# Kernel tuning notes

Hardware: AMD Instinct MI355X
Metric: run time of the kernel (lower is better)

The kernel has to match this reference:

```python
import jax, jax.numpy as jnp
import numpy as np

EMB = 256
N_HEADS = 8
N_LVLS = 4
N_POINTS = 4
HEAD_DIM = EMB // N_HEADS  # 32
D_FFN = 1024
SHAPES = [(100, 100), (50, 50), (25, 25), (13, 13)]
LEN = sum(h * w for h, w in SHAPES)  # 13294
B = 4


def setup_inputs() -> dict:
    key = jax.random.key(0)
    ks = jax.random.split(key, 20)
    rn = lambda k, s, sc=0.02: jax.random.normal(k, s, jnp.float32) * sc
    starts = np.cumsum([0] + [h * w for h, w in SHAPES])[:-1]
    return {
        'features': jax.random.normal(ks[0], (B, LEN, EMB), jnp.float32),
        'pos': jax.random.normal(ks[1], (B, LEN, EMB), jnp.float32),
        'reference_points': jax.random.uniform(ks[2], (B, LEN, N_LVLS, 2), jnp.float32),
        'spatial_shapes': jnp.array(SHAPES, jnp.int32),
        'lvl_start_idx': jnp.array(starts, jnp.int32),
        'W_off': rn(ks[3], (EMB, N_HEADS * N_LVLS * N_POINTS * 2)),
        'b_off': rn(ks[4], (N_HEADS * N_LVLS * N_POINTS * 2,), 0.5),
        'W_attn': rn(ks[5], (EMB, N_HEADS * N_LVLS * N_POINTS)),
        'b_attn': rn(ks[6], (N_HEADS * N_LVLS * N_POINTS,)),
        'W_val': rn(ks[7], (EMB, EMB)),
        'b_val': rn(ks[8], (EMB,)),
        'W_out': rn(ks[9], (EMB, EMB)),
        'b_out': rn(ks[10], (EMB,)),
        'ln1_g': jnp.ones((EMB,), jnp.float32),
        'ln1_b': jnp.zeros((EMB,), jnp.float32),
        'W1': rn(ks[11], (EMB, D_FFN)),
        'b1': rn(ks[12], (D_FFN,)),
        'W2': rn(ks[13], (D_FFN, EMB)),
        'b2': rn(ks[14], (EMB,)),
        'ln2_g': jnp.ones((EMB,), jnp.float32),
        'ln2_b': jnp.zeros((EMB,), jnp.float32),
    }


def _layer_norm(x, g, b, eps=1e-5):
    mu = jnp.mean(x, axis=-1, keepdims=True)
    var = jnp.mean(jnp.square(x - mu), axis=-1, keepdims=True)
    return (x - mu) * jax.lax.rsqrt(var + eps) * g + b


def _ms_deform_attn(q, features, reference_points, shapes, starts,
                    W_off, b_off, W_attn, b_attn, W_val, b_val, W_out, b_out):
    Bn, Lq, D = features.shape
    value = (features @ W_val + b_val).reshape(Bn, Lq, N_HEADS, HEAD_DIM)
    off = (q @ W_off + b_off).reshape(Bn, Lq, N_HEADS, N_LVLS, N_POINTS, 2)
    attn = (q @ W_attn + b_attn).reshape(Bn, Lq, N_HEADS, N_LVLS * N_POINTS)
    attn = jax.nn.softmax(attn, axis=-1).reshape(Bn, Lq, N_HEADS, N_LVLS, N_POINTS)
    # normalizer per level is (W, H) for (x, y)
    norm = jnp.array([[w, h] for h, w in shapes], jnp.float32)  # (L, 2)
    loc = reference_points[:, :, None, :, None, :] + off / norm[None, None, None, :, None, :]

    out = jnp.zeros((Bn, N_HEADS, Lq, HEAD_DIM), value.dtype)
    for l, (H_, W_) in enumerate(shapes):
        s = starts[l]
        val = value[:, s:s + H_ * W_].transpose(0, 2, 1, 3)  # (B, nH, HW, Dh)
        locl = loc[:, :, :, l]  # (B, Lq, nH, P, 2), in [0,1]
        # grid_sample align_corners=False convention
        x = locl[..., 0] * W_ - 0.5
        y = locl[..., 1] * H_ - 0.5
        x0 = jnp.floor(x); y0 = jnp.floor(y)
        wx = x - x0; wy = y - y0
        x0i = x0.astype(jnp.int32); y0i = y0.astype(jnp.int32)

        def corner(xi, yi, w):
            valid = (xi >= 0) & (xi < W_) & (yi >= 0) & (yi < H_)
            idx = jnp.clip(yi, 0, H_ - 1) * W_ + jnp.clip(xi, 0, W_ - 1)  # (B, Lq, nH, P)
            idx = idx.transpose(0, 2, 1, 3).reshape(Bn, N_HEADS, Lq * N_POINTS, 1)
            g = jnp.take_along_axis(val, idx, axis=2)  # (B, nH, Lq*P, Dh)
            wm = (w * valid.astype(w.dtype)).transpose(0, 2, 1, 3).reshape(Bn, N_HEADS, Lq * N_POINTS, 1)
            return g * wm

        samp = (corner(x0i, y0i, (1 - wx) * (1 - wy))
                + corner(x0i + 1, y0i, wx * (1 - wy))
                + corner(x0i, y0i + 1, (1 - wx) * wy)
                + corner(x0i + 1, y0i + 1, wx * wy))
        samp = samp.reshape(Bn, N_HEADS, Lq, N_POINTS, HEAD_DIM)
        aw = attn[:, :, :, l].transpose(0, 2, 1, 3)  # (B, nH, Lq, P)
        out = out + jnp.einsum('bhqpd,bhqp->bhqd', samp, aw)

    out = out.transpose(0, 2, 1, 3).reshape(Bn, Lq, D)
    return out @ W_out + b_out


def reference(features, pos, reference_points, spatial_shapes, lvl_start_idx,
              W_off, b_off, W_attn, b_attn, W_val, b_val, W_out, b_out,
              ln1_g, ln1_b, W1, b1, W2, b2, ln2_g, ln2_b):
    shapes = [tuple(int(v) for v in r) for r in np.asarray(spatial_shapes)]
    starts = [int(v) for v in np.asarray(lvl_start_idx)]
    q = features + pos
    attn_out = _ms_deform_attn(q, features, reference_points, shapes, starts,
                               W_off, b_off, W_attn, b_attn, W_val, b_val, W_out, b_out)
    x = _layer_norm(features + attn_out, ln1_g, ln1_b)  # dropout is identity in eval
    ffn = jax.nn.relu(x @ W1 + b1) @ W2 + b2
    x = _layer_norm(x + ffn, ln2_g, ln2_b)  # stochastic depth is identity in eval
    return x
```

## Files before the change

kernel.cpp:

```cpp
#include <hip/hip_runtime.h>
#include <stdint.h>

#define LEN_T 13294
#define M_TOK 53176

typedef unsigned short u16;
typedef __bf16 bf16x8 __attribute__((ext_vector_type(8)));
typedef float f32x4 __attribute__((ext_vector_type(4)));
typedef uint32_t u32x4 __attribute__((ext_vector_type(4)));

__device__ __forceinline__ u16 f2bf(float f) {
    union { float f; uint32_t u; } v; v.f = f;
    uint32_t r = v.u + 0x7fffu + ((v.u >> 16) & 1u);
    return (u16)(r >> 16);
}
__device__ __forceinline__ float bf2f(u16 s) {
    union { uint32_t u; float f; } v; v.u = ((uint32_t)s) << 16;
    return v.f;
}
__device__ __forceinline__ u16 f2h(float f) {
    union { _Float16 h; u16 u; } c; c.h = (_Float16)f; return c.u;
}
__device__ __forceinline__ float hlo(uint32_t u) {
    union { uint32_t u; _Float16 h[2]; } v; v.u = u; return (float)v.h[0];
}
__device__ __forceinline__ float hhi(uint32_t u) {
    union { uint32_t u; _Float16 h[2]; } v; v.u = u; return (float)v.h[1];
}

__device__ __forceinline__ void gload_lds16(const u16* g, u16* l) {
    __builtin_amdgcn_global_load_lds(
        (const __attribute__((address_space(1))) uint32_t*)(g),
        (__attribute__((address_space(3))) uint32_t*)(l), 16, 0, 0);
}

__global__ __launch_bounds__(256) void prep_qf(
    const float* __restrict__ feat, const float* __restrict__ pos,
    u16* __restrict__ qb, u16* __restrict__ fb, int n4)
{
    int i = blockIdx.x * blockDim.x + threadIdx.x;
    int stride = gridDim.x * blockDim.x;
    for (; i < n4; i += stride) {
        float4 f = ((const float4*)feat)[i];
        float4 p = ((const float4*)pos)[i];
        uint32_t q0 = (uint32_t)f2bf(f.x + p.x) | ((uint32_t)f2bf(f.y + p.y) << 16);
        uint32_t q1 = (uint32_t)f2bf(f.z + p.z) | ((uint32_t)f2bf(f.w + p.w) << 16);
        uint32_t f0 = (uint32_t)f2bf(f.x) | ((uint32_t)f2bf(f.y) << 16);
        uint32_t f1 = (uint32_t)f2bf(f.z) | ((uint32_t)f2bf(f.w) << 16);
        ((uint2*)qb)[i] = make_uint2(q0, q1);
        ((uint2*)fb)[i] = make_uint2(f0, f1);
    }
}

__global__ __launch_bounds__(256) void wtrans_all(
    const float* __restrict__ W_val, const float* __restrict__ W_off,
    const float* __restrict__ W_attn, const float* __restrict__ W_out,
    const float* __restrict__ W1, const float* __restrict__ W2,
    u16* __restrict__ Wt_val, u16* __restrict__ Wt_oa,
    u16* __restrict__ Wt_out, u16* __restrict__ W1f, u16* __restrict__ W2f)
{
    int gid = blockIdx.x * 256 + threadIdx.x;
    if (gid < 229376) {
        const float* W; u16* D; int K, N, off;
        if      (gid < 65536)  { W = W_val;  D = Wt_val;        K = 256; N = 256; off = gid; }
        else if (gid < 131072) { W = W_off;  D = Wt_oa;         K = 256; N = 256; off = gid - 65536; }
        else if (gid < 163840) { W = W_attn; D = Wt_oa + 65536; K = 256; N = 128; off = gid - 131072; }
        else                   { W = W_out;  D = Wt_out;        K = 256; N = 256; off = gid - 163840; }
        int n = off / K, k = off - n * K;
        D[off] = f2bf(W[(size_t)k * N + n]);
    } else if (gid < 491520) {
        int off = gid - 229376;
        int e = off & 7, lane = (off >> 3) & 63;
        int r = off >> 9;
        int ks = r & 7, ni = (r >> 3) & 1, c = r >> 4;
        int col = c * 32 + ni * 16 + (lane & 15);
        int k = ks * 32 + (lane >> 4) * 8 + e;
        W1f[off] = f2bf(W1[(size_t)k * 1024 + col]);
    } else if (gid < 753664) {
        int off = gid - 491520;
        int e = off & 7, lane = (off >> 3) & 63;
        int r = off >> 9;
        int col = (r & 15) * 16 + (lane & 15);
        int k = (r >> 4) * 32 + (lane >> 4) * 8 + e;
        W2f[off] = f2bf(W2[(size_t)k * 256 + col]);
    }
}

#define MODE_VAL 0
#define MODE_OFFATTN 1

template<int MODE>
__global__ __launch_bounds__(256, 2) void gemm128(
    const u16* __restrict__ A, const u16* __restrict__ Bt,
    int M, int K,
    const float* __restrict__ bias, const float* __restrict__ bias2,
    void* __restrict__ out0, void* __restrict__ out1)
{
    __shared__ u16 Al[128 * 64];
    __shared__ u16 Bl[128 * 64];
    const int tid = threadIdx.x;
    const int lane = tid & 63;
    const int w = tid >> 6;
    const int wr = w >> 1, wc = w & 1;
    const int m0 = blockIdx.x * 128;
    const int n0 = blockIdx.y * 128;
    const int l15 = lane & 15;
    const int kg = lane >> 4;
    const int srow = lane >> 3;
    const int scol = (lane & 7) * 8;

    f32x4 acc[4][4];
#pragma unroll
    for (int i = 0; i < 4; ++i)
#pragma unroll
        for (int j = 0; j < 4; ++j)
            acc[i][j] = (f32x4){0.f, 0.f, 0.f, 0.f};

    const int nk = K >> 6;
    for (int kc = 0; kc < nk; ++kc) {
        __syncthreads();
#pragma unroll
        for (int j = 0; j < 4; ++j) {
            int c = w * 4 + j;
            int arow = m0 + c * 8 + srow;
            arow = arow < M ? arow : M - 1;
            gload_lds16(A + (size_t)arow * K + (kc << 6) + scol, Al + c * 512);
            int brow = n0 + c * 8 + srow;
            gload_lds16(Bt + (size_t)brow * K + (kc << 6) + scol, Bl + c * 512);
        }
        __syncthreads();
#pragma unroll
        for (int ks = 0; ks < 2; ++ks) {
            bf16x8 af[4], bfr[4];
#pragma unroll
            for (int i = 0; i < 4; ++i) {
                af[i]  = *(const bf16x8*)(Al + (wr * 64 + i * 16 + l15) * 64 + ks * 32 + kg * 8);
                bfr[i] = *(const bf16x8*)(Bl + (wc * 64 + i * 16 + l15) * 64 + ks * 32 + kg * 8);
            }
#pragma unroll
            for (int mi = 0; mi < 4; ++mi)
#pragma unroll
                for (int ni = 0; ni < 4; ++ni)
                    acc[mi][ni] = __builtin_amdgcn_mfma_f32_16x16x32_bf16(
                        af[mi], bfr[ni], acc[mi][ni], 0, 0, 0);
        }
    }

#pragma unroll
    for (int mi = 0; mi < 4; ++mi) {
#pragma unroll
        for (int r = 0; r < 4; ++r) {
            int row = m0 + wr * 64 + mi * 16 + kg * 4 + r;
            if (row >= M) continue;
#pragma unroll
            for (int ni = 0; ni < 4; ++ni) {
                int col = n0 + wc * 64 + ni * 16 + l15;
                float v = acc[mi][ni][r];
                if (MODE == MODE_VAL) {
                    int bI = row / LEN_T;
                    int t = row - bI * LEN_T;
                    int hh = col >> 5, d = col & 31;
                    ((u16*)out0)[((size_t)(bI * 8 + hh) * LEN_T + t) * 32 + d] =
                        f2h(v + bias[col]);
                } else {
                    if (col < 256) {
                        ((float*)out0)[((size_t)(col >> 5) * M_TOK + row) * 32 + (col & 31)] =
                            v + bias[col];
                    } else {
                        int c = col - 256;
                        ((float*)out1)[((size_t)(c >> 4) * M_TOK + row) * 16 + (c & 15)] =
                            v + bias2[c];
                    }
                }
            }
        }
    }
}

template<int KSTEPS, int OUTF32>
__global__ __launch_bounds__(256, 2) void gemm_ln(
    const u16* __restrict__ A, const u16* __restrict__ Bt,
    const float* __restrict__ bias, const u16* __restrict__ res,
    const float* __restrict__ g, const float* __restrict__ bb,
    u16* __restrict__ outb, float* __restrict__ outf, int M)
{
    __shared__ char ldsraw[66560];
    u16* Al = (u16*)ldsraw;
    u16* Bl = (u16*)(ldsraw + 8192);
    float* dump = (float*)ldsraw;
    const int tid = threadIdx.x;
    const int lane = tid & 63;
    const int w = tid >> 6;
    const int l15 = lane & 15;
    const int kg = lane >> 4;
    const int srow = lane >> 3;
    const int scol = (lane & 7) * 8;
    const int m0 = blockIdx.x * 64;
    const int K = KSTEPS * 64;

    f32x4 acc[4][4];
#pragma unroll
    for (int i = 0; i < 4; ++i)
#pragma unroll
        for (int j = 0; j < 4; ++j)
            acc[i][j] = (f32x4){0.f, 0.f, 0.f, 0.f};

    for (int kc = 0; kc < KSTEPS; ++kc) {
        __syncthreads();
#pragma unroll
        for (int j = 0; j < 2; ++j) {
            int c = w * 2 + j;
            int arow = m0 + c * 8 + srow;
            arow = arow < M ? arow : M - 1;
            gload_lds16(A + (size_t)arow * K + (kc << 6) + scol, Al + c * 512);
        }
#pragma unroll
        for (int j = 0; j < 8; ++j) {
            int c = w * 8 + j;
            int brow = c * 8 + srow;
            gload_lds16(Bt + (size_t)brow * K + (kc << 6) + scol, Bl + c * 512);
        }
        __syncthreads();
#pragma unroll
        for (int ks = 0; ks < 2; ++ks) {
            bf16x8 af[4], bfr[4];
#pragma unroll
            for (int i = 0; i < 4; ++i) {
                af[i]  = *(const bf16x8*)(Al + (i * 16 + l15) * 64 + ks * 32 + kg * 8);
                bfr[i] = *(const bf16x8*)(Bl + (w * 64 + i * 16 + l15) * 64 + ks * 32 + kg * 8);
            }
#pragma unroll
            for (int mi = 0; mi < 4; ++mi)
#pragma unroll
                for (int ni = 0; ni < 4; ++ni)
                    acc[mi][ni] = __builtin_amdgcn_mfma_f32_16x16x32_bf16(
                        af[mi], bfr[ni], acc[mi][ni], 0, 0, 0);
        }
    }

    __syncthreads();
#pragma unroll
    for (int mi = 0; mi < 4; ++mi) {
#pragma unroll
        for (int r = 0; r < 4; ++r) {
            int rr = mi * 16 + kg * 4 + r;
            int gr = m0 + rr; gr = gr < M ? gr : M - 1;
#pragma unroll
            for (int ni = 0; ni < 4; ++ni) {
                int col = w * 64 + ni * 16 + l15;
                dump[rr * 260 + col] = acc[mi][ni][r] + bias[col] +
                                       bf2f(res[(size_t)gr * 256 + col]);
            }
        }
    }
    __syncthreads();

    float4 gv = *(const float4*)(g + lane * 4);
    float4 bv = *(const float4*)(bb + lane * 4);
#pragma unroll
    for (int i = 0; i < 16; ++i) {
        int rr = w * 16 + i;
        float4 x = *(const float4*)(dump + rr * 260 + lane * 4);
        float s1 = x.x + x.y + x.z + x.w;
        float s2 = x.x*x.x + x.y*x.y + x.z*x.z + x.w*x.w;
#pragma unroll
        for (int o = 1; o < 64; o <<= 1) {
            s1 += __shfl_xor(s1, o);
            s2 += __shfl_xor(s2, o);
        }
        float mu = s1 * (1.0f / 256.0f);
        float var = s2 * (1.0f / 256.0f) - mu * mu;
        float rs = rsqrtf(var + 1e-5f);
        float o0 = (x.x - mu) * rs * gv.x + bv.x;
        float o1 = (x.y - mu) * rs * gv.y + bv.y;
        float o2 = (x.z - mu) * rs * gv.z + bv.z;
        float o3 = (x.w - mu) * rs * gv.w + bv.w;
        int grow = m0 + rr;
        if (grow < M) {
            if (OUTF32) {
                *(float4*)(outf + (size_t)grow * 256 + lane * 4) =
                    make_float4(o0, o1, o2, o3);
            } else {
                uint32_t u0 = (uint32_t)f2bf(o0) | ((uint32_t)f2bf(o1) << 16);
                uint32_t u1 = (uint32_t)f2bf(o2) | ((uint32_t)f2bf(o3) << 16);
                *(uint2*)(outb + (size_t)grow * 256 + lane * 4) = make_uint2(u0, u1);
            }
        }
    }
}

__global__ __launch_bounds__(256, 2) void ffn_fused(
    const u16* __restrict__ A, const u16* __restrict__ W1f, const u16* __restrict__ W2f,
    const float* __restrict__ b1, const float* __restrict__ b2,
    const float* __restrict__ g, const float* __restrict__ bb,
    float* __restrict__ outf, int M)
{
    __shared__ char lds[66560];
    u16* Axl = (u16*)lds;
    u16* ht  = (u16*)(lds + 33792);
    float* dump = (float*)lds;
    const int tid = threadIdx.x;
    const int lane = tid & 63;
    const int w = tid >> 6;
    const int l15 = lane & 15;
    const int kg = lane >> 4;
    const int m0 = blockIdx.x * 64;

#pragma unroll
    for (int i = 0; i < 8; ++i) {
        int linear = i * 256 + tid;
        int row = linear >> 5;
        int gcol = (linear & 31) * 8;
        int grow = m0 + row; grow = grow < M ? grow : M - 1;
        uint4 v = *(const uint4*)(A + (size_t)grow * 256 + gcol);
        *(uint4*)(Axl + row * 264 + gcol) = v;
    }
    __syncthreads();

    f32x4 acc[4][4];
#pragma unroll
    for (int i = 0; i < 4; ++i)
#pragma unroll
        for (int j = 0; j < 4; ++j)
            acc[i][j] = (f32x4){0.f, 0.f, 0.f, 0.f};

    for (int hc = 0; hc < 8; ++hc) {
        f32x4 acc2[4][2];
#pragma unroll
        for (int i = 0; i < 4; ++i) {
            acc2[i][0] = (f32x4){0.f, 0.f, 0.f, 0.f};
            acc2[i][1] = (f32x4){0.f, 0.f, 0.f, 0.f};
        }
#pragma unroll
        for (int ks = 0; ks < 8; ++ks) {
            bf16x8 af[4], bw[2];
#pragma unroll
            for (int ni = 0; ni < 2; ++ni)
                bw[ni] = *(const bf16x8*)(W1f +
                    ((size_t)((((hc * 4 + w) * 2 + ni) * 8 + ks)) << 9) + lane * 8);
#pragma unroll
            for (int mi = 0; mi < 4; ++mi)
                af[mi] = *(const bf16x8*)(Axl + (mi * 16 + l15) * 264 + ks * 32 + kg * 8);
#pragma unroll
            for (int mi = 0; mi < 4; ++mi)
#pragma unroll
                for (int ni = 0; ni < 2; ++ni)
                    acc2[mi][ni] = __builtin_amdgcn_mfma_f32_16x16x32_bf16(
                        af[mi], bw[ni], acc2[mi][ni], 0, 0, 0);
        }
        __syncthreads();
#pragma unroll
        for (int mi = 0; mi < 4; ++mi) {
#pragma unroll
            for (int ni = 0; ni < 2; ++ni) {
#pragma unroll
                for (int r = 0; r < 4; ++r) {
                    int rr = mi * 16 + kg * 4 + r;
                    int cl = w * 32 + ni * 16 + l15;
                    float hv = acc2[mi][ni][r] + b1[hc * 128 + cl];
                    ht[rr * 136 + cl] = f2bf(hv > 0.f ? hv : 0.f);
                }
            }
        }
        __syncthreads();
#pragma unroll
        for (int ks2 = 0; ks2 < 4; ++ks2) {
            bf16x8 ah[4], bw2[4];
#pragma unroll
            for (int ni = 0; ni < 4; ++ni)
                bw2[ni] = *(const bf16x8*)(W2f +
                    ((size_t)(((hc * 4 + ks2) * 16 + w * 4 + ni)) << 9) + lane * 8);
#pragma unroll
            for (int mi = 0; mi < 4; ++mi)
                ah[mi] = *(const bf16x8*)(ht + (mi * 16 + l15) * 136 + ks2 * 32 + kg * 8);
#pragma unroll
            for (int mi = 0; mi < 4; ++mi)
#pragma unroll
                for (int ni = 0; ni < 4; ++ni)
                    acc[mi][ni] = __builtin_amdgcn_mfma_f32_16x16x32_bf16(
                        ah[mi], bw2[ni], acc[mi][ni], 0, 0, 0);
        }
    }

    __syncthreads();
#pragma unroll
    for (int mi = 0; mi < 4; ++mi) {
#pragma unroll
        for (int r = 0; r < 4; ++r) {
            int rr = mi * 16 + kg * 4 + r;
            int gr = m0 + rr; gr = gr < M ? gr : M - 1;
#pragma unroll
            for (int ni = 0; ni < 4; ++ni) {
                int col = w * 64 + ni * 16 + l15;
                dump[rr * 260 + col] = acc[mi][ni][r] + b2[col] +
                                       bf2f(A[(size_t)gr * 256 + col]);
            }
        }
    }
    __syncthreads();

    float4 gv = *(const float4*)(g + lane * 4);
    float4 bv = *(const float4*)(bb + lane * 4);
#pragma unroll
    for (int i = 0; i < 16; ++i) {
        int rr = w * 16 + i;
        float4 x = *(const float4*)(dump + rr * 260 + lane * 4);
        float s1 = x.x + x.y + x.z + x.w;
        float s2 = x.x*x.x + x.y*x.y + x.z*x.z + x.w*x.w;
#pragma unroll
        for (int o = 1; o < 64; o <<= 1) {
            s1 += __shfl_xor(s1, o);
            s2 += __shfl_xor(s2, o);
        }
        float mu = s1 * (1.0f / 256.0f);
        float var = s2 * (1.0f / 256.0f) - mu * mu;
        float rs = rsqrtf(var + 1e-5f);
        float o0 = (x.x - mu) * rs * gv.x + bv.x;
        float o1 = (x.y - mu) * rs * gv.y + bv.y;
        float o2 = (x.z - mu) * rs * gv.z + bv.z;
        float o3 = (x.w - mu) * rs * gv.w + bv.w;
        int grow = m0 + rr;
        if (grow < M) {
            *(float4*)(outf + (size_t)grow * 256 + lane * 4) =
                make_float4(o0, o1, o2, o3);
        }
    }
}

__device__ __forceinline__ void acc8h(u32x4 v, float w, float* acc) {
    acc[0] = fmaf(hlo(v.x), w, acc[0]);
    acc[1] = fmaf(hhi(v.x), w, acc[1]);
    acc[2] = fmaf(hlo(v.y), w, acc[2]);
    acc[3] = fmaf(hhi(v.y), w, acc[3]);
    acc[4] = fmaf(hlo(v.z), w, acc[4]);
    acc[5] = fmaf(hhi(v.z), w, acc[5]);
    acc[6] = fmaf(hlo(v.w), w, acc[6]);
    acc[7] = fmaf(hhi(v.w), w, acc[7]);
}

__global__ __launch_bounds__(256, 4) void sample_kernel(
    const float* __restrict__ offt, const float* __restrict__ attnt,
    const u16* __restrict__ value, const float* __restrict__ refp,
    u16* __restrict__ samp)
{
    int bid = blockIdx.x;
    int lb  = (bid & 7) * 832 + (bid >> 3);
    int bh  = lb / 208;
    int tblk = lb - bh * 208;
    int pr  = threadIdx.x >> 2;
    int dq  = threadIdx.x & 3;
    int tok = tblk * 64 + pr;
    if (tok >= LEN_T) return;
    int b = bh >> 3, h = bh & 7;
    size_t row = (size_t)b * LEN_T + tok;

    const f32x4* ap = (const f32x4*)(attnt + ((size_t)h * M_TOK + row) * 16);
    float aw[16];
#pragma unroll
    for (int i = 0; i < 4; ++i) {
        f32x4 v = __builtin_nontemporal_load(ap + i);
        aw[4*i+0] = v.x; aw[4*i+1] = v.y; aw[4*i+2] = v.z; aw[4*i+3] = v.w;
    }
    float mx = -1e30f;
#pragma unroll
    for (int i = 0; i < 16; ++i) mx = fmaxf(mx, aw[i]);
    float ssum = 0.f;
#pragma unroll
    for (int i = 0; i < 16; ++i) { aw[i] = __expf(aw[i] - mx); ssum += aw[i]; }
    float inv = 1.0f / ssum;
#pragma unroll
    for (int i = 0; i < 16; ++i) aw[i] *= inv;

    const f32x4* rp4 = (const f32x4*)(refp + row * 8);
    f32x4 r01 = __builtin_nontemporal_load(rp4);
    f32x4 r23 = __builtin_nontemporal_load(rp4 + 1);
    float rxy[8] = {r01.x, r01.y, r01.z, r01.w, r23.x, r23.y, r23.z, r23.w};

    float acc[8];
#pragma unroll
    for (int d = 0; d < 8; ++d) acc[d] = 0.f;

    const f32x4* op4 = (const f32x4*)(offt + ((size_t)h * M_TOK + row) * 32);

    const int Wl[4] = {100, 50, 25, 13};
    const int Sl[4] = {0, 10000, 12500, 13125};

#pragma unroll
    for (int l = 0; l < 4; ++l) {
        const int W_ = Wl[l];
        const float Wf = (float)W_;
        const float invW = 1.0f / Wf;
        const u16* vb = value + ((size_t)bh * LEN_T + Sl[l]) * 32 + dq * 8;
        float rx = rxy[l*2+0], ry = rxy[l*2+1];
        f32x4 o0 = __builtin_nontemporal_load(op4 + l*2);
        f32x4 o1 = __builtin_nontemporal_load(op4 + l*2 + 1);
        float dxs[4] = {o0.x, o0.z, o1.x, o1.z};
        float dys[4] = {o0.y, o0.w, o1.y, o1.w};
        float wts[16];
        int   offs[16];
#pragma unroll
        for (int p = 0; p < 4; ++p) {
            float x = fmaf(fmaf(dxs[p], invW, rx), Wf, -0.5f);
            float y = fmaf(fmaf(dys[p], invW, ry), Wf, -0.5f);
            float x0f = floorf(x), y0f = floorf(y);
            int x0 = (int)x0f, y0 = (int)y0f;
            int x1 = x0 + 1, y1 = y0 + 1;
            float wx = x - x0f, wy = y - y0f;
            float vx0 = ((unsigned)x0 < (unsigned)W_) ? 1.f : 0.f;
            float vx1 = ((unsigned)x1 < (unsigned)W_) ? 1.f : 0.f;
            float vy0 = ((unsigned)y0 < (unsigned)W_) ? 1.f : 0.f;
            float vy1 = ((unsigned)y1 < (unsigned)W_) ? 1.f : 0.f;
            int cx0 = min(max(x0, 0), W_ - 1);
            int cx1 = min(max(x1, 0), W_ - 1);
            int cy0 = min(max(y0, 0), W_ - 1);
            int cy1 = min(max(y1, 0), W_ - 1);
            float a = aw[l*4 + p];
            wts[p*4+0] = (1.f - wx) * (1.f - wy) * a * vx0 * vy0;
            wts[p*4+1] = wx * (1.f - wy) * a * vx1 * vy0;
            wts[p*4+2] = (1.f - wx) * wy * a * vx0 * vy1;
            wts[p*4+3] = wx * wy * a * vx1 * vy1;
            offs[p*4+0] = (cy0 * W_ + cx0) * 32;
            offs[p*4+1] = (cy0 * W_ + cx1) * 32;
            offs[p*4+2] = (cy1 * W_ + cx0) * 32;
            offs[p*4+3] = (cy1 * W_ + cx1) * 32;
        }
        u32x4 vv[16];
#pragma unroll
        for (int i = 0; i < 16; ++i)
            vv[i] = *(const u32x4*)(vb + offs[i]);
#pragma unroll
        for (int i = 0; i < 16; ++i)
            acc8h(vv[i], wts[i], acc);
    }
    u32x4 uo;
    uo.x = (uint32_t)f2bf(acc[0]) | ((uint32_t)f2bf(acc[1]) << 16);
    uo.y = (uint32_t)f2bf(acc[2]) | ((uint32_t)f2bf(acc[3]) << 16);
    uo.z = (uint32_t)f2bf(acc[4]) | ((uint32_t)f2bf(acc[5]) << 16);
    uo.w = (uint32_t)f2bf(acc[6]) | ((uint32_t)f2bf(acc[7]) << 16);
    __builtin_nontemporal_store(uo, (u32x4*)(samp + row * 256 + h * 32 + dq * 8));
}

extern "C" void kernel_launch(void* const* d_in, const int* in_sizes, int n_in,
                              void* d_out, int out_size, void* d_ws, size_t ws_size,
                              hipStream_t stream)
{
    const float* features = (const float*)d_in[0];
    const float* pos      = (const float*)d_in[1];
    const float* refp     = (const float*)d_in[2];
    const float* W_off  = (const float*)d_in[5];
    const float* b_off  = (const float*)d_in[6];
    const float* W_attn = (const float*)d_in[7];
    const float* b_attn = (const float*)d_in[8];
    const float* W_val  = (const float*)d_in[9];
    const float* b_val  = (const float*)d_in[10];
    const float* W_out  = (const float*)d_in[11];
    const float* b_out  = (const float*)d_in[12];
    const float* ln1_g  = (const float*)d_in[13];
    const float* ln1_b  = (const float*)d_in[14];
    const float* W1     = (const float*)d_in[15];
    const float* b1     = (const float*)d_in[16];
    const float* W2     = (const float*)d_in[17];
    const float* b2     = (const float*)d_in[18];
    const float* ln2_g  = (const float*)d_in[19];
    const float* ln2_b  = (const float*)d_in[20];
    float* out = (float*)d_out;

    char* ws = (char*)d_ws;
    size_t o = 0;
    auto alloc = [&](size_t bytes) { char* p = ws + o; o += (bytes + 255) & ~(size_t)255; return p; };
    u16* Wt_val = (u16*)alloc((size_t)256 * 256 * 2);
    u16* Wt_oa  = (u16*)alloc((size_t)384 * 256 * 2);
    u16* Wt_out = (u16*)alloc((size_t)256 * 256 * 2);
    u16* W1f    = (u16*)alloc((size_t)1024 * 256 * 2);
    u16* W2f    = (u16*)alloc((size_t)256 * 1024 * 2);
    u16* qb     = (u16*)alloc((size_t)M_TOK * 256 * 2);
    u16* fb     = (u16*)alloc((size_t)M_TOK * 256 * 2);
    char* big   = alloc((size_t)M_TOK * 1024 * 2);
    u16*   value = (u16*)big;
    float* offt  = (float*)(big + (size_t)M_TOK * 256 * 2);
    float* attnt = (float*)(big + (size_t)M_TOK * 256 * 2 + (size_t)M_TOK * 256 * 4);
    u16* samp = qb;
    u16* xb   = qb;

    dim3 blk(256);
    const int mb  = (M_TOK + 127) / 128;
    const int mb64 = (M_TOK + 63) / 64;

    prep_qf<<<2048, blk, 0, stream>>>(features, pos, qb, fb, M_TOK * 256 / 4);
    wtrans_all<<<2944, blk, 0, stream>>>(W_val, W_off, W_attn, W_out, W1, W2,
                                         Wt_val, Wt_oa, Wt_out, W1f, W2f);

    gemm128<MODE_VAL><<<dim3(mb, 2), blk, 0, stream>>>(
        fb, Wt_val, M_TOK, 256, b_val, nullptr, value, nullptr);
    gemm128<MODE_OFFATTN><<<dim3(mb, 3), blk, 0, stream>>>(
        qb, Wt_oa, M_TOK, 256, b_off, b_attn, offt, attnt);

    sample_kernel<<<6656, blk, 0, stream>>>(offt, attnt, value, refp, samp);

    gemm_ln<4, 0><<<mb64, blk, 0, stream>>>(
        samp, Wt_out, b_out, fb, ln1_g, ln1_b, xb, nullptr, M_TOK);

    ffn_fused<<<mb64, blk, 0, stream>>>(
        xb, W1f, W2f, b1, b2, ln2_g, ln2_b, out, M_TOK);
}
```

Measured before the change: 375.4 us.

## Store offsets/attention logits as fp16 and widen per-thread channel slice in sampler

The offset/attention projection GEMM now writes its outputs as fp16 instead of fp32, halving the intermediate write and the sampler's read traffic. The sampler now reads the packed half values and assigns 16 channels per thread (2 threads per token-head) instead of 8, halving the grid and the number of threads that redo the softmax and coordinate math. The cost is reduced precision of sampling offsets, which can shift bilinear positions on the 100-wide level, plus higher register use per thread.

```diff
diff --git a/kernel.cpp b/kernel.cpp
--- a/kernel.cpp
+++ b/kernel.cpp
@@ -164,12 +164,12 @@
                         f2h(v + bias[col]);
                 } else {
                     if (col < 256) {
-                        ((float*)out0)[((size_t)(col >> 5) * M_TOK + row) * 32 + (col & 31)] =
-                            v + bias[col];
+                        ((u16*)out0)[((size_t)(col >> 5) * M_TOK + row) * 32 + (col & 31)] =
+                            f2h(v + bias[col]);
                     } else {
                         int c = col - 256;
-                        ((float*)out1)[((size_t)(c >> 4) * M_TOK + row) * 16 + (c & 15)] =
-                            v + bias2[c];
+                        ((u16*)out1)[((size_t)(c >> 4) * M_TOK + row) * 16 + (c & 15)] =
+                            f2h(v + bias2[c]);
                     }
                 }
             }
@@ -439,28 +439,29 @@
 }
 
 __global__ __launch_bounds__(256, 4) void sample_kernel(
-    const float* __restrict__ offt, const float* __restrict__ attnt,
+    const u16* __restrict__ offt, const u16* __restrict__ attnt,
     const u16* __restrict__ value, const float* __restrict__ refp,
     u16* __restrict__ samp)
 {
     int bid = blockIdx.x;
-    int lb  = (bid & 7) * 832 + (bid >> 3);
-    int bh  = lb / 208;
-    int tblk = lb - bh * 208;
-    int pr  = threadIdx.x >> 2;
-    int dq  = threadIdx.x & 3;
-    int tok = tblk * 64 + pr;
+    int lb  = (bid & 7) * 416 + (bid >> 3);
+    int bh  = lb / 104;
+    int tblk = lb - bh * 104;
+    int pr  = threadIdx.x >> 1;
+    int dq  = threadIdx.x & 1;
+    int tok = tblk * 128 + pr;
     if (tok >= LEN_T) return;
     int b = bh >> 3, h = bh & 7;
     size_t row = (size_t)b * LEN_T + tok;
 
-    const f32x4* ap = (const f32x4*)(attnt + ((size_t)h * M_TOK + row) * 16);
+    const u32x4* ap = (const u32x4*)(attnt + ((size_t)h * M_TOK + row) * 16);
+    u32x4 a0 = __builtin_nontemporal_load(ap);
+    u32x4 a1 = __builtin_nontemporal_load(ap + 1);
     float aw[16];
-#pragma unroll
-    for (int i = 0; i < 4; ++i) {
-        f32x4 v = __builtin_nontemporal_load(ap + i);
-        aw[4*i+0] = v.x; aw[4*i+1] = v.y; aw[4*i+2] = v.z; aw[4*i+3] = v.w;
-    }
+    aw[0]=hlo(a0.x); aw[1]=hhi(a0.x); aw[2]=hlo(a0.y); aw[3]=hhi(a0.y);
+    aw[4]=hlo(a0.z); aw[5]=hhi(a0.z); aw[6]=hlo(a0.w); aw[7]=hhi(a0.w);
+    aw[8]=hlo(a1.x); aw[9]=hhi(a1.x); aw[10]=hlo(a1.y); aw[11]=hhi(a1.y);
+    aw[12]=hlo(a1.z); aw[13]=hhi(a1.z); aw[14]=hlo(a1.w); aw[15]=hhi(a1.w);
     float mx = -1e30f;
 #pragma unroll
     for (int i = 0; i < 16; ++i) mx = fmaxf(mx, aw[i]);
@@ -476,11 +477,11 @@
     f32x4 r23 = __builtin_nontemporal_load(rp4 + 1);
     float rxy[8] = {r01.x, r01.y, r01.z, r01.w, r23.x, r23.y, r23.z, r23.w};
 
-    float acc[8];
-#pragma unroll
-    for (int d = 0; d < 8; ++d) acc[d] = 0.f;
-
-    const f32x4* op4 = (const f32x4*)(offt + ((size_t)h * M_TOK + row) * 32);
+    float acc[16];
+#pragma unroll
+    for (int d = 0; d < 16; ++d) acc[d] = 0.f;
+
+    const u32x4* op4 = (const u32x4*)(offt + ((size_t)h * M_TOK + row) * 32);
 
     const int Wl[4] = {100, 50, 25, 13};
     const int Sl[4] = {0, 10000, 12500, 13125};
@@ -490,12 +491,11 @@
         const int W_ = Wl[l];
         const float Wf = (float)W_;
         const float invW = 1.0f / Wf;
-        const u16* vb = value + ((size_t)bh * LEN_T + Sl[l]) * 32 + dq * 8;
+        const u16* vb = value + ((size_t)bh * LEN_T + Sl[l]) * 32 + dq * 16;
         float rx = rxy[l*2+0], ry = rxy[l*2+1];
-        f32x4 o0 = __builtin_nontemporal_load(op4 + l*2);
-        f32x4 o1 = __builtin_nontemporal_load(op4 + l*2 + 1);
-        float dxs[4] = {o0.x, o0.z, o1.x, o1.z};
-        float dys[4] = {o0.y, o0.w, o1.y, o1.w};
+        u32x4 ov = __builtin_nontemporal_load(op4 + l);
+        float dxs[4] = {hlo(ov.x), hlo(ov.y), hlo(ov.z), hlo(ov.w)};
+        float dys[4] = {hhi(ov.x), hhi(ov.y), hhi(ov.z), hhi(ov.w)};
         float wts[16];
         int   offs[16];
 #pragma unroll
@@ -524,20 +524,34 @@
             offs[p*4+2] = (cy1 * W_ + cx0) * 32;
             offs[p*4+3] = (cy1 * W_ + cx1) * 32;
         }
-        u32x4 vv[16];
-#pragma unroll
-        for (int i = 0; i < 16; ++i)
-            vv[i] = *(const u32x4*)(vb + offs[i]);
-#pragma unroll
-        for (int i = 0; i < 16; ++i)
-            acc8h(vv[i], wts[i], acc);
-    }
-    u32x4 uo;
-    uo.x = (uint32_t)f2bf(acc[0]) | ((uint32_t)f2bf(acc[1]) << 16);
-    uo.y = (uint32_t)f2bf(acc[2]) | ((uint32_t)f2bf(acc[3]) << 16);
-    uo.z = (uint32_t)f2bf(acc[4]) | ((uint32_t)f2bf(acc[5]) << 16);
-    uo.w = (uint32_t)f2bf(acc[6]) | ((uint32_t)f2bf(acc[7]) << 16);
-    __builtin_nontemporal_store(uo, (u32x4*)(samp + row * 256 + h * 32 + dq * 8));
+#pragma unroll
+        for (int c2 = 0; c2 < 2; ++c2) {
+            u32x4 va[8], vb8[8];
+#pragma unroll
+            for (int i = 0; i < 8; ++i) {
+                const u16* p = vb + offs[c2*8 + i];
+                va[i]  = *(const u32x4*)(p);
+                vb8[i] = *(const u32x4*)(p + 8);
+            }
+#pragma unroll
+            for (int i = 0; i < 8; ++i) {
+                acc8h(va[i],  wts[c2*8 + i], acc);
+                acc8h(vb8[i], wts[c2*8 + i], acc + 8);
+            }
+        }
+    }
+    u32x4 uo0, uo1;
+    uo0.x = (uint32_t)f2bf(acc[0])  | ((uint32_t)f2bf(acc[1])  << 16);
+    uo0.y = (uint32_t)f2bf(acc[2])  | ((uint32_t)f2bf(acc[3])  << 16);
+    uo0.z = (uint32_t)f2bf(acc[4])  | ((uint32_t)f2bf(acc[5])  << 16);
+    uo0.w = (uint32_t)f2bf(acc[6])  | ((uint32_t)f2bf(acc[7])  << 16);
+    uo1.x = (uint32_t)f2bf(acc[8])  | ((uint32_t)f2bf(acc[9])  << 16);
+    uo1.y = (uint32_t)f2bf(acc[10]) | ((uint32_t)f2bf(acc[11]) << 16);
+    uo1.z = (uint32_t)f2bf(acc[12]) | ((uint32_t)f2bf(acc[13]) << 16);
+    uo1.w = (uint32_t)f2bf(acc[14]) | ((uint32_t)f2bf(acc[15]) << 16);
+    u32x4* sp = (u32x4*)(samp + row * 256 + h * 32 + dq * 16);
+    __builtin_nontemporal_store(uo0, sp);
+    __builtin_nontemporal_store(uo1, sp + 1);
 }
 
 extern "C" void kernel_launch(void* const* d_in, const int* in_sizes, int n_in,
@@ -576,9 +590,9 @@
     u16* qb     = (u16*)alloc((size_t)M_TOK * 256 * 2);
     u16* fb     = (u16*)alloc((size_t)M_TOK * 256 * 2);
     char* big   = alloc((size_t)M_TOK * 1024 * 2);
-    u16*   value = (u16*)big;
-    float* offt  = (float*)(big + (size_t)M_TOK * 256 * 2);
-    float* attnt = (float*)(big + (size_t)M_TOK * 256 * 2 + (size_t)M_TOK * 256 * 4);
+    u16* value  = (u16*)big;
+    u16* offt   = (u16*)(big + (size_t)M_TOK * 256 * 2);
+    u16* attnt  = (u16*)(big + (size_t)M_TOK * 256 * 2 * 2);
     u16* samp = qb;
     u16* xb   = qb;
 
@@ -595,7 +609,7 @@
     gemm128<MODE_OFFATTN><<<dim3(mb, 3), blk, 0, stream>>>(
         qb, Wt_oa, M_TOK, 256, b_off, b_attn, offt, attnt);
 
-    sample_kernel<<<6656, blk, 0, stream>>>(offt, attnt, value, refp, samp);
+    sample_kernel<<<3328, blk, 0, stream>>>(offt, attnt, value, refp, samp);
 
     gemm_ln<4, 0><<<mb64, blk, 0, stream>>>(
         samp, Wt_out, b_out, fb, ln1_g, ln1_b, xb, nullptr, M_TOK);
```

Measured after the change: 564.9 us. +50.5%, slower.
